# Kernel optimization log

Measured on AMD Instinct MI355X. Metric: run time of the kernel, lower is better.

## Reference

```python
import jax, jax.numpy as jnp
import numpy as np

NUM_HEADS = 2
POOL_K = 256
REPEAT = 20


def setup_inputs() -> dict:
    key = jax.random.key(0)
    k1, k2, k3 = jax.random.split(key, 3)
    C = 6144
    d = C // NUM_HEADS                      # 3072
    N = REPEAT * (d // POOL_K)              # 240, required by Pq add
    x = jax.random.normal(k1, (N, C), dtype=jnp.float32)
    w_qkv = jax.random.normal(k2, (3 * C, C), dtype=jnp.float32) * 0.02
    w_proj = jax.random.normal(k3, (C, C), dtype=jnp.float32) * 0.02
    b_proj = jnp.zeros((C,), dtype=jnp.float32)
    return {"x": x, "w_qkv": w_qkv, "w_proj": w_proj, "b_proj": b_proj}


def reference(x, w_qkv, w_proj, b_proj):
    N, C = x.shape
    H = NUM_HEADS
    d = C // H
    scale = d ** -0.5
    # qkv: (N, 3C) -> (N, 3, H, d) -> (3, H, N, d)
    qkv = (x @ w_qkv.T).reshape(N, 3, H, d).transpose(1, 2, 0, 3)
    q, k, v = qkv[0], qkv[1], qkv[2]        # each (H, N, d)
    # MaxPool1d(256) over last dim, then tile x20 along last dim -> (H, N, N)
    Pq = q.reshape(H, N, d // POOL_K, POOL_K).max(axis=-1)
    Pq = jnp.tile(Pq, (1, 1, REPEAT))       # (H, N, N)
    attn = jnp.einsum('hnd,hmd->hnm', q, k) * scale + 0.1 * Pq
    attn = jax.nn.softmax(attn, axis=-1)
    out = jnp.einsum('hnm,hmd->hnd', attn, v)    # (H, N, d)
    out = out.transpose(1, 0, 2).reshape(N, C)
    return out @ w_proj.T + b_proj
```

## Files before the change

kernel.cpp:

```cpp
#include <hip/hip_runtime.h>
#include <hip/hip_bf16.h>

#define NN 240
#define CC 6144
#define DD 3072
#define C3 18432
#define HH 2

typedef __attribute__((ext_vector_type(8))) short bf16x8;
typedef __attribute__((ext_vector_type(4))) float f32x4;
typedef unsigned short ushort_t;

static __device__ __forceinline__ unsigned short f2bf(float f) {
    __hip_bfloat16 h = __float2bfloat16(f);
    return __builtin_bit_cast(unsigned short, h);
}

#define GLDS16(g, l) __builtin_amdgcn_global_load_lds( \
    (const __attribute__((address_space(1))) void*)(g), \
    (__attribute__((address_space(3))) void*)(l), 16, 0, 0)

__global__ __launch_bounds__(256, 2)
void gemm_t(const ushort_t* __restrict__ Ab, int lda, long long sAz,
            const float* __restrict__ B, int ldb, long long sBz,
            const float* __restrict__ bias,
            float* __restrict__ C0, long long sC0z,
            float* __restrict__ CP, long long sCPz,
            int ldc, int N, int Kc, int KS) {
    __shared__ ushort_t sA[2][256 * 32];
    __shared__ float    sB[2][128 * 32];

    const int zc = blockIdx.z;
    const int z = zc / KS, kc = zc % KS;
    const ushort_t* Abase = Ab + (size_t)z * sAz + (size_t)kc * Kc;
    const float*    Bbase = B  + (size_t)z * sBz + (size_t)kc * Kc;
    float* Cw = (kc == 0) ? (C0 + (size_t)z * sC0z)
                          : (CP + (size_t)(z * (KS - 1) + kc - 1) * sCPz);

    const int n0 = blockIdx.x * 128;
    const int tid = threadIdx.x, lane = tid & 63, wid = tid >> 6;
    const int l16 = lane & 15, lk = lane >> 4;

    const int ar = lane >> 2;
    const int akoct = (lane & 3) ^ ((lane >> 3) & 3);

    long long bofs[4];
#pragma unroll
    for (int i = 0; i < 4; ++i) {
        int cl = (wid * 4 + i) * 8 + (lane >> 3);
        int cg = n0 + cl; if (cg > N - 1) cg = N - 1;
        bofs[i] = (long long)cg * ldb + ((lane & 7) ^ ((lane >> 3) & 7)) * 4;
    }

    const int nt = Kc / 32;
    f32x4 acc[4][8] = {};

    auto ISSUE = [&](int t, int par) {
        ushort_t* sa = par ? sA[1] : sA[0];
        float*    sb = par ? sB[1] : sB[0];
#pragma unroll
        for (int i = 0; i < 4; ++i) {
            int rb = (wid * 4 + i) * 16;
            GLDS16(Abase + (size_t)(rb + ar) * lda + akoct * 8 + (size_t)t * 32,
                   sa + rb * 32);
        }
#pragma unroll
        for (int i = 0; i < 4; ++i) {
            int cb = (wid * 4 + i) * 8;
            GLDS16(Bbase + bofs[i] + (size_t)t * 32, sb + cb * 32);
        }
    };

    auto COMPUTE = [&](int par) {
        const char* As = par ? (const char*)sA[1] : (const char*)sA[0];
        const char* Bs = par ? (const char*)sB[1] : (const char*)sB[0];
        bf16x8 af[4];
#pragma unroll
        for (int mt = 0; mt < 4; ++mt) {
            int r = wid * 64 + mt * 16 + l16;
            af[mt] = *(const bf16x8*)(As + r * 64
                        + ((lk ^ ((r >> 1) & 3)) * 16));
        }
#pragma unroll
        for (int nf = 0; nf < 8; ++nf) {
            int c = nf * 16 + l16;
            const char* cb = Bs + c * 128;
            f32x4 lo = *(const f32x4*)(cb + (((2 * lk) ^ (c & 7)) * 16));
            f32x4 hi = *(const f32x4*)(cb + (((2 * lk + 1) ^ (c & 7)) * 16));
            bf16x8 r;
            r[0] = (short)f2bf(lo[0]); r[1] = (short)f2bf(lo[1]);
            r[2] = (short)f2bf(lo[2]); r[3] = (short)f2bf(lo[3]);
            r[4] = (short)f2bf(hi[0]); r[5] = (short)f2bf(hi[1]);
            r[6] = (short)f2bf(hi[2]); r[7] = (short)f2bf(hi[3]);
            __builtin_amdgcn_s_setprio(1);
#pragma unroll
            for (int mt = 0; mt < 4; ++mt)
                acc[mt][nf] = __builtin_amdgcn_mfma_f32_16x16x32_bf16(
                    af[mt], r, acc[mt][nf], 0, 0, 0);
            __builtin_amdgcn_s_setprio(0);
        }
    };

    ISSUE(0, 0);
    for (int t = 0; t < nt; ++t) {
        int tn = (t + 1 < nt) ? t + 1 : t;
        ISSUE(tn, (t + 1) & 1);
        asm volatile("s_waitcnt vmcnt(8)" ::: "memory");
        __builtin_amdgcn_sched_barrier(0);
        __builtin_amdgcn_s_barrier();
        COMPUTE(t & 1);
        __builtin_amdgcn_sched_barrier(0);
        __builtin_amdgcn_s_barrier();
    }

#pragma unroll
    for (int mt = 0; mt < 4; ++mt) {
#pragma unroll
        for (int j = 0; j < 4; ++j) {
            int grow = wid * 64 + mt * 16 + lk * 4 + j;
            if (grow < NN) {
#pragma unroll
                for (int nf = 0; nf < 8; ++nf) {
                    int gcol = n0 + nf * 16 + l16;
                    if (gcol < N) {
                        float v = acc[mt][nf][j];
                        if (kc == 0 && bias) v += bias[gcol];
                        Cw[(size_t)grow * ldc + gcol] = v;
                    }
                }
            }
        }
    }
}

__global__ __launch_bounds__(256)
void convert_kernel(const float* __restrict__ x, ushort_t* __restrict__ xb) {
    int id = blockIdx.x * 256 + threadIdx.x;
    int row = id / 768, c8 = id % 768;
    bf16x8 o = {};
    if (row < NN) {
        const float* p = x + (size_t)row * CC + c8 * 8;
        float4 a = *(const float4*)p, b = *(const float4*)(p + 4);
        o[0] = (short)f2bf(a.x); o[1] = (short)f2bf(a.y);
        o[2] = (short)f2bf(a.z); o[3] = (short)f2bf(a.w);
        o[4] = (short)f2bf(b.x); o[5] = (short)f2bf(b.y);
        o[6] = (short)f2bf(b.z); o[7] = (short)f2bf(b.w);
    }
    *(bf16x8*)(xb + (size_t)row * CC + c8 * 8) = o;
}

__global__ __launch_bounds__(256)
void reduce_qkv(float4* __restrict__ q4, const float4* __restrict__ p4,
                long long s4, ushort_t* __restrict__ qb) {
    int i = blockIdx.x * 256 + threadIdx.x;
    float4 a = q4[i];
#pragma unroll
    for (int k = 0; k < 3; ++k) {
        float4 b = p4[(size_t)k * s4 + i];
        a.x += b.x; a.y += b.y; a.z += b.z; a.w += b.w;
    }
    q4[i] = a;
    int row = i / 4608, c4 = i % 4608;
    if (c4 < 1536) {
        ushort4 u;
        u.x = f2bf(a.x); u.y = f2bf(a.y); u.z = f2bf(a.z); u.w = f2bf(a.w);
        *(ushort4*)(qb + (size_t)row * CC + c4 * 4) = u;
    }
}

__global__ __launch_bounds__(256)
void reduce_proj(float4* __restrict__ o4, const float4* __restrict__ p4,
                 long long s4) {
    int i = blockIdx.x * 256 + threadIdx.x;
    float4 a = o4[i];
#pragma unroll
    for (int k = 0; k < 11; ++k) {
        float4 b = p4[(size_t)k * s4 + i];
        a.x += b.x; a.y += b.y; a.z += b.z; a.w += b.w;
    }
    o4[i] = a;
}

__global__ __launch_bounds__(256)
void qmax_kernel(const float* __restrict__ qkv, float* __restrict__ qmax) {
    int idx = blockIdx.x * 4 + (threadIdx.x >> 6);
    int lane = threadIdx.x & 63;
    int c = idx % 12;
    int r = idx / 12;
    int n = r % NN, h = r / NN;
    const float* p = qkv + (size_t)n * C3 + h * DD + c * 256 + lane * 4;
    float4 f = *(const float4*)p;
    float m = fmaxf(fmaxf(f.x, f.y), fmaxf(f.z, f.w));
#pragma unroll
    for (int off = 32; off >= 1; off >>= 1)
        m = fmaxf(m, __shfl_xor(m, off));
    if (lane == 0) qmax[idx] = m;
}

__global__ __launch_bounds__(256)
void softmax_kernel(float* __restrict__ attn, const float* __restrict__ gpart,
                    int ksm1, const float* __restrict__ qmax) {
    int r = blockIdx.x * 4 + (threadIdx.x >> 6);
    int lane = threadIdx.x & 63;
    int z = r / NN, n = r % NN;
    float* row = attn + (size_t)r * NN;
    const float* qm = qmax + r * 12;
    const float scale = 0.0180421959f;
    float v[4];
    float mx = -1e30f;
#pragma unroll
    for (int i = 0; i < 4; ++i) {
        int m = lane + 64 * i;
        v[i] = -1e30f;
        if (m < NN) {
            float s = row[m];
            for (int kc = 0; kc < ksm1; ++kc)
                s += gpart[(size_t)(z * ksm1 + kc) * (NN * NN)
                           + (size_t)n * NN + m];
            v[i] = s * scale + 0.1f * qm[m % 12];
        }
        mx = fmaxf(mx, v[i]);
    }
#pragma unroll
    for (int off = 32; off >= 1; off >>= 1)
        mx = fmaxf(mx, __shfl_xor(mx, off));
    float s = 0.f;
#pragma unroll
    for (int i = 0; i < 4; ++i) {
        v[i] = __expf(v[i] - mx);
        s += v[i];
    }
#pragma unroll
    for (int off = 32; off >= 1; off >>= 1)
        s += __shfl_xor(s, off);
    float inv = 1.0f / s;
#pragma unroll
    for (int i = 0; i < 4; ++i) {
        int m = lane + 64 * i;
        if (m < NN) row[m] = v[i] * inv;
    }
}

__global__ __launch_bounds__(256)
void pv_kernel(const float* __restrict__ attn, const float* __restrict__ qkv,
               ushort_t* __restrict__ preb) {
    const int h = blockIdx.z;
    const int n0 = blockIdx.y * 16;
    const int dd0 = blockIdx.x * 256;
    __shared__ float s_attn[16 * NN];
    for (int i = threadIdx.x; i < 16 * NN; i += 256)
        s_attn[i] = attn[(size_t)h * NN * NN + (n0 + i / NN) * NN + (i % NN)];
    __syncthreads();

    const float* vp = qkv + 2 * CC + h * DD + dd0 + threadIdx.x;
    float acc[16] = {};
    for (int m = 0; m < NN; m += 4) {
        float v0 = vp[(size_t)(m + 0) * C3];
        float v1 = vp[(size_t)(m + 1) * C3];
        float v2 = vp[(size_t)(m + 2) * C3];
        float v3 = vp[(size_t)(m + 3) * C3];
#pragma unroll
        for (int i = 0; i < 16; ++i) {
            float4 a = *(const float4*)&s_attn[i * NN + m];
            acc[i] += a.x * v0 + a.y * v1 + a.z * v2 + a.w * v3;
        }
    }
#pragma unroll
    for (int i = 0; i < 16; ++i)
        preb[(size_t)(n0 + i) * CC + h * DD + dd0 + threadIdx.x] =
            f2bf(acc[i]);
}

extern "C" void kernel_launch(void* const* d_in, const int* in_sizes, int n_in,
                              void* d_out, int out_size, void* d_ws, size_t ws_size,
                              hipStream_t stream) {
    const float* x      = (const float*)d_in[0];
    const float* w_qkv  = (const float*)d_in[1];
    const float* w_proj = (const float*)d_in[2];
    const float* b_proj = (const float*)d_in[3];
    float* out = (float*)d_out;

    const size_t f_qkv  = (size_t)NN * C3;
    const size_t f_attn = (size_t)HH * NN * NN;
    const size_t f_qmax = (size_t)HH * NN * 12;
    const size_t f_pre  = (size_t)NN * CC;
    float* qkv   = (float*)d_ws;
    float* attn  = qkv + f_qkv;
    float* qmaxb = attn + f_attn;
    ushort_t* xb   = (ushort_t*)(qmaxb + f_qmax);
    ushort_t* qb   = xb + (size_t)256 * CC;
    ushort_t* preb = qb + (size_t)256 * CC;
    float* gpart = (float*)(preb + (size_t)256 * CC);

    convert_kernel<<<768, 256, 0, stream>>>(x, xb);

    gemm_t<<<dim3(C3 / 128, 1, 4), 256, 0, stream>>>(
        xb, CC, 0LL, w_qkv, CC, 0LL, nullptr,
        qkv, 0LL, gpart, (long long)f_qkv,
        C3, C3, CC / 4, 4);
    reduce_qkv<<<4320, 256, 0, stream>>>((float4*)qkv, (const float4*)gpart,
        (long long)(f_qkv / 4), qb);

    qmax_kernel<<<1440, 256, 0, stream>>>(qkv, qmaxb);

    gemm_t<<<dim3(2, 1, HH * 24), 256, 0, stream>>>(
        qb, CC, (long long)DD,
        qkv + CC, C3, (long long)DD, nullptr,
        attn, (long long)(NN * NN), gpart, (long long)(NN * NN),
        NN, NN, DD / 24, 24);

    softmax_kernel<<<120, 256, 0, stream>>>(attn, gpart, 23, qmaxb);

    pv_kernel<<<dim3(12, 15, HH), 256, 0, stream>>>(attn, qkv, preb);

    gemm_t<<<dim3(CC / 128, 1, 12), 256, 0, stream>>>(
        preb, CC, 0LL, w_proj, CC, 0LL, b_proj,
        out, 0LL, gpart, (long long)f_pre,
        CC, CC, CC / 12, 12);
    reduce_proj<<<1440, 256, 0, stream>>>((float4*)out, (const float4*)gpart,
        (long long)(f_pre / 4));
}
```

Before: 380.4 us.

## Shrink GEMM N-tile to 64, drop double buffering, reduce split-K factors

The GEMM kernel now uses a 64-column output tile with single-buffered LDS and plain __syncthreads, replacing the double-buffered pipeline with its manual waitcnt, sched barriers and setprio. Occupancy is raised to 4 blocks per CU. Split-K drops from 4 to 2 for QKV and from 12 to 8 for the projection, and the reduce kernels shrink to match. The aim is more blocks, less partial-sum traffic and cheaper reductions, at the cost of losing the overlap between global loads and MFMA compute.

```diff
diff --git a/kernel.cpp b/kernel.cpp
--- a/kernel.cpp
+++ b/kernel.cpp
@@ -20,15 +20,15 @@
     (const __attribute__((address_space(1))) void*)(g), \
     (__attribute__((address_space(3))) void*)(l), 16, 0, 0)
 
-__global__ __launch_bounds__(256, 2)
-void gemm_t(const ushort_t* __restrict__ Ab, int lda, long long sAz,
-            const float* __restrict__ B, int ldb, long long sBz,
-            const float* __restrict__ bias,
-            float* __restrict__ C0, long long sC0z,
-            float* __restrict__ CP, long long sCPz,
-            int ldc, int N, int Kc, int KS) {
-    __shared__ ushort_t sA[2][256 * 32];
-    __shared__ float    sB[2][128 * 32];
+__global__ __launch_bounds__(256, 4)
+void gemm_m97(const ushort_t* __restrict__ Ab, int lda, long long sAz,
+              const float* __restrict__ B, int ldb, long long sBz,
+              const float* __restrict__ bias,
+              float* __restrict__ C0, long long sC0z,
+              float* __restrict__ CP, long long sCPz,
+              int ldc, int N, int Kc, int KS) {
+    __shared__ ushort_t sA[256 * 32];
+    __shared__ float    sB[64 * 32];
 
     const int zc = blockIdx.z;
     const int z = zc / KS, kc = zc % KS;
@@ -37,54 +37,49 @@
     float* Cw = (kc == 0) ? (C0 + (size_t)z * sC0z)
                           : (CP + (size_t)(z * (KS - 1) + kc - 1) * sCPz);
 
-    const int n0 = blockIdx.x * 128;
+    const int n0 = blockIdx.x * 64;
     const int tid = threadIdx.x, lane = tid & 63, wid = tid >> 6;
     const int l16 = lane & 15, lk = lane >> 4;
 
     const int ar = lane >> 2;
     const int akoct = (lane & 3) ^ ((lane >> 3) & 3);
 
-    long long bofs[4];
-#pragma unroll
-    for (int i = 0; i < 4; ++i) {
-        int cl = (wid * 4 + i) * 8 + (lane >> 3);
+    long long bofs[2];
+#pragma unroll
+    for (int i = 0; i < 2; ++i) {
+        int cl = (wid * 2 + i) * 8 + (lane >> 3);
         int cg = n0 + cl; if (cg > N - 1) cg = N - 1;
         bofs[i] = (long long)cg * ldb + ((lane & 7) ^ ((lane >> 3) & 7)) * 4;
     }
 
     const int nt = Kc / 32;
-    f32x4 acc[4][8] = {};
-
-    auto ISSUE = [&](int t, int par) {
-        ushort_t* sa = par ? sA[1] : sA[0];
-        float*    sb = par ? sB[1] : sB[0];
+    f32x4 acc[4][4] = {};
+
+    for (int t = 0; t < nt; ++t) {
 #pragma unroll
         for (int i = 0; i < 4; ++i) {
             int rb = (wid * 4 + i) * 16;
             GLDS16(Abase + (size_t)(rb + ar) * lda + akoct * 8 + (size_t)t * 32,
-                   sa + rb * 32);
-        }
-#pragma unroll
-        for (int i = 0; i < 4; ++i) {
-            int cb = (wid * 4 + i) * 8;
-            GLDS16(Bbase + bofs[i] + (size_t)t * 32, sb + cb * 32);
-        }
-    };
-
-    auto COMPUTE = [&](int par) {
-        const char* As = par ? (const char*)sA[1] : (const char*)sA[0];
-        const char* Bs = par ? (const char*)sB[1] : (const char*)sB[0];
+                   sA + rb * 32);
+        }
+#pragma unroll
+        for (int i = 0; i < 2; ++i) {
+            int cb = (wid * 2 + i) * 8;
+            GLDS16(Bbase + bofs[i] + (size_t)t * 32, sB + cb * 32);
+        }
+        __syncthreads();
+
         bf16x8 af[4];
 #pragma unroll
         for (int mt = 0; mt < 4; ++mt) {
             int r = wid * 64 + mt * 16 + l16;
-            af[mt] = *(const bf16x8*)(As + r * 64
+            af[mt] = *(const bf16x8*)((const char*)sA + r * 64
                         + ((lk ^ ((r >> 1) & 3)) * 16));
         }
 #pragma unroll
-        for (int nf = 0; nf < 8; ++nf) {
+        for (int nf = 0; nf < 4; ++nf) {
             int c = nf * 16 + l16;
-            const char* cb = Bs + c * 128;
+            const char* cb = (const char*)sB + c * 128;
             f32x4 lo = *(const f32x4*)(cb + (((2 * lk) ^ (c & 7)) * 16));
             f32x4 hi = *(const f32x4*)(cb + (((2 * lk + 1) ^ (c & 7)) * 16));
             bf16x8 r;
@@ -92,25 +87,12 @@
             r[2] = (short)f2bf(lo[2]); r[3] = (short)f2bf(lo[3]);
             r[4] = (short)f2bf(hi[0]); r[5] = (short)f2bf(hi[1]);
             r[6] = (short)f2bf(hi[2]); r[7] = (short)f2bf(hi[3]);
-            __builtin_amdgcn_s_setprio(1);
 #pragma unroll
             for (int mt = 0; mt < 4; ++mt)
                 acc[mt][nf] = __builtin_amdgcn_mfma_f32_16x16x32_bf16(
                     af[mt], r, acc[mt][nf], 0, 0, 0);
-            __builtin_amdgcn_s_setprio(0);
-        }
-    };
-
-    ISSUE(0, 0);
-    for (int t = 0; t < nt; ++t) {
-        int tn = (t + 1 < nt) ? t + 1 : t;
-        ISSUE(tn, (t + 1) & 1);
-        asm volatile("s_waitcnt vmcnt(8)" ::: "memory");
-        __builtin_amdgcn_sched_barrier(0);
-        __builtin_amdgcn_s_barrier();
-        COMPUTE(t & 1);
-        __builtin_amdgcn_sched_barrier(0);
-        __builtin_amdgcn_s_barrier();
+        }
+        __syncthreads();
     }
 
 #pragma unroll
@@ -120,7 +102,7 @@
             int grow = wid * 64 + mt * 16 + lk * 4 + j;
             if (grow < NN) {
 #pragma unroll
-                for (int nf = 0; nf < 8; ++nf) {
+                for (int nf = 0; nf < 4; ++nf) {
                     int gcol = n0 + nf * 16 + l16;
                     if (gcol < N) {
                         float v = acc[mt][nf][j];
@@ -151,14 +133,10 @@
 
 __global__ __launch_bounds__(256)
 void reduce_qkv(float4* __restrict__ q4, const float4* __restrict__ p4,
-                long long s4, ushort_t* __restrict__ qb) {
+                ushort_t* __restrict__ qb) {
     int i = blockIdx.x * 256 + threadIdx.x;
-    float4 a = q4[i];
-#pragma unroll
-    for (int k = 0; k < 3; ++k) {
-        float4 b = p4[(size_t)k * s4 + i];
-        a.x += b.x; a.y += b.y; a.z += b.z; a.w += b.w;
-    }
+    float4 a = q4[i], b = p4[i];
+    a.x += b.x; a.y += b.y; a.z += b.z; a.w += b.w;
     q4[i] = a;
     int row = i / 4608, c4 = i % 4608;
     if (c4 < 1536) {
@@ -174,7 +152,7 @@
     int i = blockIdx.x * 256 + threadIdx.x;
     float4 a = o4[i];
 #pragma unroll
-    for (int k = 0; k < 11; ++k) {
+    for (int k = 0; k < 7; ++k) {
         float4 b = p4[(size_t)k * s4 + i];
         a.x += b.x; a.y += b.y; a.z += b.z; a.w += b.w;
     }
@@ -294,16 +272,15 @@
 
     convert_kernel<<<768, 256, 0, stream>>>(x, xb);
 
-    gemm_t<<<dim3(C3 / 128, 1, 4), 256, 0, stream>>>(
+    gemm_m97<<<dim3(C3 / 64, 1, 2), 256, 0, stream>>>(
         xb, CC, 0LL, w_qkv, CC, 0LL, nullptr,
         qkv, 0LL, gpart, (long long)f_qkv,
-        C3, C3, CC / 4, 4);
-    reduce_qkv<<<4320, 256, 0, stream>>>((float4*)qkv, (const float4*)gpart,
-        (long long)(f_qkv / 4), qb);
+        C3, C3, CC / 2, 2);
+    reduce_qkv<<<4320, 256, 0, stream>>>((float4*)qkv, (const float4*)gpart, qb);
 
     qmax_kernel<<<1440, 256, 0, stream>>>(qkv, qmaxb);
 
-    gemm_t<<<dim3(2, 1, HH * 24), 256, 0, stream>>>(
+    gemm_m97<<<dim3(4, 1, HH * 24), 256, 0, stream>>>(
         qb, CC, (long long)DD,
         qkv + CC, C3, (long long)DD, nullptr,
         attn, (long long)(NN * NN), gpart, (long long)(NN * NN),
@@ -313,10 +290,10 @@
 
     pv_kernel<<<dim3(12, 15, HH), 256, 0, stream>>>(attn, qkv, preb);
 
-    gemm_t<<<dim3(CC / 128, 1, 12), 256, 0, stream>>>(
+    gemm_m97<<<dim3(CC / 64, 1, 8), 256, 0, stream>>>(
         preb, CC, 0LL, w_proj, CC, 0LL, b_proj,
         out, 0LL, gpart, (long long)f_pre,
-        CC, CC, CC / 12, 12);
+        CC, CC, CC / 8, 8);
     reduce_proj<<<1440, 256, 0, stream>>>((float4*)out, (const float4*)gpart,
         (long long)(f_pre / 4));
 }
```

Measured after the change: 369.0 us. 3.0% less time.
